# Performance work log

Measured on AMD Instinct MI355X. Metric: run time of the kernel, lower is better.

## Reference

```python
import jax, jax.numpy as jnp
import numpy as np

H = 4  # num_heads in all three MultiheadAttention layers


def _mha(x, valid, Wq, Wk, Wv, Wo, bq, bk, bv, bo):
    """Batched self-attention with key_padding_mask, matching torch MHA math.
    x: [..., L, D]; valid: [..., L] float (1=real token, 0=pad)."""
    lead = x.shape[:-2]
    L, D = x.shape[-2], x.shape[-1]
    dh = D // H
    q = (x @ Wq + bq).reshape(*lead, L, H, dh)
    k = (x @ Wk + bk).reshape(*lead, L, H, dh)
    v = (x @ Wv + bv).reshape(*lead, L, H, dh)
    scores = jnp.einsum('...qhd,...khd->...hqk', q, k) / jnp.sqrt(jnp.asarray(dh, x.dtype))
    neg = jnp.asarray(-1e9, x.dtype)  # finite so fully-masked rows stay NaN-free
    scores = jnp.where(valid[..., None, None, :] > 0, scores, neg)
    a = jax.nn.softmax(scores, axis=-1)
    o = jnp.einsum('...hqk,...khd->...qhd', a, v).reshape(*lead, L, D)
    return o @ Wo + bo


def _masked_mean(x, m):
    # (x * m).sum over sequence / (m.sum + 1e-10); fully-masked -> exact zeros,
    # matching the torch zeros() fallback branch.
    mm = m[..., None]
    return (x * mm).sum(-2) / (mm.sum(-2) + 1e-10)


def setup_inputs() -> dict:
    key = jax.random.key(0)
    B, S, N, W, D = 16, 8, 16, 64, 256
    ks = jax.random.split(key, 16)
    inp = {
        'word_embeddings': jax.random.normal(ks[0], (B, S, N, W, D), dtype=jnp.float32),
        'attention_mask': jax.random.randint(ks[1], (B, S, N, W), 0, 2).astype(jnp.int32),
    }
    i = 2
    for lvl in 'wsc':  # word / sentence / section attention params
        for p in ('Wq', 'Wk', 'Wv', 'Wo'):
            inp[lvl + p] = 0.02 * jax.random.normal(ks[i], (D, D), dtype=jnp.float32)
            i += 1
        for p in ('bq', 'bk', 'bv', 'bo'):
            inp[lvl + p] = jnp.zeros((D,), jnp.float32)
    return inp


def reference(word_embeddings, attention_mask,
              wWq, wWk, wWv, wWo, wbq, wbk, wbv, wbo,
              sWq, sWk, sWv, sWo, sbq, sbk, sbv, sbo,
              cWq, cWk, cWv, cWo, cbq, cbk, cbv, cbo):
    dt = word_embeddings.dtype
    mask = attention_mask.astype(dt)                       # [B,S,N,W]
    # word level: attention within each sentence, then masked mean pooling
    wo = _mha(word_embeddings, mask, wWq, wWk, wWv, wWo, wbq, wbk, wbv, wbo)
    sent = _masked_mean(wo, mask)                          # [B,S,N,D]
    # sentence level
    sent_mask = (mask.sum(-1) > 0).astype(dt)              # [B,S,N]
    so = _mha(sent, sent_mask, sWq, sWk, sWv, sWo, sbq, sbk, sbv, sbo)
    sec = _masked_mean(so, sent_mask)                      # [B,S,D]
    # section level
    sec_mask = (mask.sum((-1, -2)) > 0).astype(dt)         # [B,S]
    co = _mha(sec, sec_mask, cWq, cWk, cWv, cWo, cbq, cbk, cbv, cbo)
    doc = _masked_mean(co, sec_mask)                       # [B,D]
    return doc
```

## Files before the change

kernel.cpp:

```cpp
#include <hip/hip_runtime.h>

constexpr int D = 256;

typedef __attribute__((ext_vector_type(8))) __bf16 bf16x8;
typedef __attribute__((ext_vector_type(4))) float f32x4;
typedef __attribute__((ext_vector_type(16))) float f32x16;

__device__ inline unsigned short f2b(float f) {
    unsigned u = __builtin_bit_cast(unsigned, f);
    u = (u + 0x7fffu + ((u >> 16) & 1u)) >> 16;
    return (unsigned short)u;
}
__device__ inline unsigned cvt_pk_bf16(float lo, float hi) {
    unsigned r;
    asm volatile("v_cvt_pk_bf16_f32 %0, %1, %2" : "=v"(r) : "v"(lo), "v"(hi));
    return r;
}
__device__ inline bf16x8 ld_frag(const void* p) {
    uint4 r = *(const uint4*)p;
    return __builtin_bit_cast(bf16x8, r);
}
__device__ inline bf16x8 mk_frag(unsigned d0, unsigned d1, unsigned d2, unsigned d3) {
    uint4 r = {d0, d1, d2, d3};
    return __builtin_bit_cast(bf16x8, r);
}
template<int CTRL>
__device__ inline float dpp_f(float v) {
    return __builtin_bit_cast(float,
        __builtin_amdgcn_update_dpp(0, __builtin_bit_cast(int, v), CTRL, 0xf, 0xf, true));
}
__device__ inline float rsum16(float v) {
    v += dpp_f<0x121>(v);
    v += dpp_f<0x122>(v);
    v += dpp_f<0x124>(v);
    v += dpp_f<0x128>(v);
    return v;
}
__device__ inline float rmax16(float v) {
    v = fmaxf(v, dpp_f<0x121>(v));
    v = fmaxf(v, dpp_f<0x122>(v));
    v = fmaxf(v, dpp_f<0x124>(v));
    v = fmaxf(v, dpp_f<0x128>(v));
    return v;
}
constexpr float CE = 0.125f * 1.44269504f;

__global__ void prep_wt3(const float* __restrict__ q0, const float* __restrict__ k0,
                         const float* __restrict__ q1, const float* __restrict__ k1,
                         const float* __restrict__ q2, const float* __restrict__ k2,
                         unsigned short* __restrict__ WT) {
    const int b = blockIdx.x, k = threadIdx.x;
    const int lvl = b >> 9, c = b & 511;
    const float* Wq = (lvl == 0) ? q0 : (lvl == 1) ? q1 : q2;
    const float* Wk = (lvl == 0) ? k0 : (lvl == 1) ? k1 : k2;
    const float* W = (c < 256) ? Wq : Wk;
    WT[(size_t)b * 256 + k] = f2b(W[k * 256 + (c & 255)]);
}

__global__ __launch_bounds__(512, 4)
void word_attn(const float* __restrict__ X, const int* __restrict__ Mask,
               const unsigned short* __restrict__ WT,
               const float* __restrict__ bq, const float* __restrict__ bk,
               float* __restrict__ Zout, float* __restrict__ Cnt)
{
    __shared__ unsigned short sX[64 * 256];
    __shared__ unsigned short sK[64 * 256];
    __shared__ float sM[64];
    __shared__ float sAbarT[64][4];
    __shared__ float sCt;

    const int tid = threadIdx.x;
    const int blk = blockIdx.x;
    const float* Xs = X + (size_t)blk * 64 * D;
    char* sXb = (char*)sX;
    char* sKb = (char*)sK;
    const int lane = tid & 63, w = tid >> 6;
    const int l31 = lane & 31, hi = lane >> 5;

    {
        const float4* X4 = (const float4*)Xs;
        float4 xv[8];
        #pragma unroll
        for (int j = 0; j < 8; ++j) xv[j] = X4[tid + j * 512];
        if (tid < 64) sM[tid] = (float)Mask[(size_t)blk * 64 + tid];
        #pragma unroll
        for (int j = 0; j < 8; ++j) {
            uint2 p;
            p.x = cvt_pk_bf16(xv[j].x, xv[j].y);
            p.y = cvt_pk_bf16(xv[j].z, xv[j].w);
            const int row = w + 8 * j;
            *(uint2*)(sXb + row * 512 + ((lane * 8) ^ ((row & 7) << 4))) = p;
        }
    }
    const unsigned short* wtp = WT + (size_t)(w * 64 + l31) * 256 + hi * 8;
    bf16x8 aA[2], aB[2], aC[2], aD[2], b0[2], b1[2];
#define LDA(buf, kkv) { buf[0] = ld_frag(wtp + (kkv) * 16); buf[1] = ld_frag(wtp + 8192 + (kkv) * 16); }
#define LDB(buf, kkv) { \
        buf[0] = ld_frag(sXb + l31 * 512 + (((kkv) * 32 + hi * 16) ^ ((l31 & 7) << 4))); \
        buf[1] = ld_frag(sXb + (32 + l31) * 512 + (((kkv) * 32 + hi * 16) ^ ((l31 & 7) << 4))); }
    LDA(aA, 0); LDA(aB, 1); LDA(aC, 2);
    __syncthreads();
    if (tid < 64) {
        float v = sM[tid];
        #pragma unroll
        for (int o = 1; o < 64; o <<= 1) v += __shfl_xor(v, o);
        if (tid == 0) sCt = v;
    }

    f32x16 acc[2][2];
    {
        const float* bias = (w < 4) ? bq : bk;
        const int fb = (w & 3) * 64;
        #pragma unroll
        for (int mf = 0; mf < 2; ++mf)
            #pragma unroll
            for (int g = 0; g < 4; ++g) {
                float4 b4 = *(const float4*)(bias + fb + mf * 32 + 8 * g + 4 * hi);
                #pragma unroll
                for (int nt = 0; nt < 2; ++nt) {
                    acc[mf][nt][4 * g + 0] = b4.x;
                    acc[mf][nt][4 * g + 1] = b4.y;
                    acc[mf][nt][4 * g + 2] = b4.z;
                    acc[mf][nt][4 * g + 3] = b4.w;
                }
            }
#define MFMA4(a, b) { \
        acc[0][0] = __builtin_amdgcn_mfma_f32_32x32x16_bf16(a[0], b[0], acc[0][0], 0, 0, 0); \
        acc[0][1] = __builtin_amdgcn_mfma_f32_32x32x16_bf16(a[0], b[1], acc[0][1], 0, 0, 0); \
        acc[1][0] = __builtin_amdgcn_mfma_f32_32x32x16_bf16(a[1], b[0], acc[1][0], 0, 0, 0); \
        acc[1][1] = __builtin_amdgcn_mfma_f32_32x32x16_bf16(a[1], b[1], acc[1][1], 0, 0, 0); }
#define PSTEP(ab, bb, an, ka, bn, kb, da, db) { \
        if (da) LDA(an, ka); \
        if (db) LDB(bn, kb); \
        __builtin_amdgcn_s_setprio(1); \
        MFMA4(ab, bb); \
        __builtin_amdgcn_s_setprio(0); }
        LDB(b0, 0);
        PSTEP(aA, b0, aD,  3, b1,  1, 1, 1);
        PSTEP(aB, b1, aA,  4, b0,  2, 1, 1);
        PSTEP(aC, b0, aB,  5, b1,  3, 1, 1);
        PSTEP(aD, b1, aC,  6, b0,  4, 1, 1);
        PSTEP(aA, b0, aD,  7, b1,  5, 1, 1);
        PSTEP(aB, b1, aA,  8, b0,  6, 1, 1);
        PSTEP(aC, b0, aB,  9, b1,  7, 1, 1);
        PSTEP(aD, b1, aC, 10, b0,  8, 1, 1);
        PSTEP(aA, b0, aD, 11, b1,  9, 1, 1);
        PSTEP(aB, b1, aA, 12, b0, 10, 1, 1);
        PSTEP(aC, b0, aB, 13, b1, 11, 1, 1);
        PSTEP(aD, b1, aC, 14, b0, 12, 1, 1);
        PSTEP(aA, b0, aD, 15, b1, 13, 1, 1);
        PSTEP(aB, b1, aA,  0, b0, 14, 0, 1);
        PSTEP(aC, b0, aB,  0, b1, 15, 0, 1);
        PSTEP(aD, b1, aC,  0, b0,  0, 0, 0);
    }

    bf16x8 qfrag[4][2];
    if (w < 4) {
        #pragma unroll
        for (int kk = 0; kk < 4; ++kk) {
            const int mf = kk >> 1, r0 = 8 * (kk & 1);
            #pragma unroll
            for (int i = 0; i < 2; ++i)
                qfrag[kk][i] = mk_frag(
                    cvt_pk_bf16(acc[mf][i][r0 + 0], acc[mf][i][r0 + 1]),
                    cvt_pk_bf16(acc[mf][i][r0 + 2], acc[mf][i][r0 + 3]),
                    cvt_pk_bf16(acc[mf][i][r0 + 4], acc[mf][i][r0 + 5]),
                    cvt_pk_bf16(acc[mf][i][r0 + 6], acc[mf][i][r0 + 7]));
        }
    } else {
        #pragma unroll
        for (int nt = 0; nt < 2; ++nt) {
            const int t = nt * 32 + l31;
            char* rowp = sKb + t * 512;
            const int sw = (t & 7) << 4;
            #pragma unroll
            for (int mf = 0; mf < 2; ++mf)
                #pragma unroll
                for (int g = 0; g < 4; ++g) {
                    uint2 v;
                    v.x = cvt_pk_bf16(acc[mf][nt][4 * g + 0], acc[mf][nt][4 * g + 1]);
                    v.y = cvt_pk_bf16(acc[mf][nt][4 * g + 2], acc[mf][nt][4 * g + 3]);
                    const int fbyte = (w & 3) * 128 + 64 * mf + 32 * (g >> 1) + 16 * hi + 8 * (g & 1);
                    *(uint2*)(rowp + (fbyte ^ sw)) = v;
                }
        }
    }
    __syncthreads();

    if (w < 4) {
        const int h = w;
        f32x16 sc00 = {}, sc01 = {}, sc10 = {}, sc11 = {};
        #pragma unroll
        for (int kk = 0; kk < 4; ++kk) {
            const int fby = h * 128 + kk * 32 + hi * 16;
            bf16x8 kb0 = ld_frag(sKb + l31 * 512 + (fby ^ ((l31 & 7) << 4)));
            bf16x8 kb1 = ld_frag(sKb + (32 + l31) * 512 + (fby ^ ((l31 & 7) << 4)));
            __builtin_amdgcn_s_setprio(1);
            sc00 = __builtin_amdgcn_mfma_f32_32x32x16_bf16(qfrag[kk][0], kb0, sc00, 0, 0, 0);
            sc01 = __builtin_amdgcn_mfma_f32_32x32x16_bf16(qfrag[kk][0], kb1, sc01, 0, 0, 0);
            sc10 = __builtin_amdgcn_mfma_f32_32x32x16_bf16(qfrag[kk][1], kb0, sc10, 0, 0, 0);
            sc11 = __builtin_amdgcn_mfma_f32_32x32x16_bf16(qfrag[kk][1], kb1, sc11, 0, 0, 0);
            __builtin_amdgcn_s_setprio(0);
        }
        const bool k0ok = sM[l31] > 0.f, k1ok = sM[32 + l31] > 0.f;
        float pm0 = 0.f, pm1 = 0.f;
#define SMROW(SC0, SC1, itile) { \
        _Pragma("unroll") \
        for (int r = 0; r < 16; ++r) { \
            const int qrow = 32 * (itile) + (r & 3) + 8 * (r >> 2) + 4 * hi; \
            float e0 = k0ok ? __builtin_amdgcn_exp2f(SC0[r] * CE) : 0.f; \
            float e1 = k1ok ? __builtin_amdgcn_exp2f(SC1[r] * CE) : 0.f; \
            float se = rsum16(e0 + e1); \
            se += __shfl_xor(se, 16); \
            const float wr = sM[qrow] * __builtin_amdgcn_rcpf(se); \
            pm0 += e0 * wr; pm1 += e1 * wr; } }
        SMROW(sc00, sc01, 0)
        SMROW(sc10, sc11, 1)
#undef SMROW
        pm0 += __shfl_xor(pm0, 32);
        pm1 += __shfl_xor(pm1, 32);
        if (hi == 0) {
            sAbarT[l31][h] = pm0;
            sAbarT[32 + l31][h] = pm1;
        }
    }
    uint2 xz[8];
    #pragma unroll
    for (int j = 0; j < 8; ++j) {
        const int t = w + 8 * j;
        xz[j] = *(const uint2*)(sXb + t * 512 + ((lane * 8) ^ ((t & 7) << 4)));
    }
    __syncthreads();

    float zp[4][4];
    #pragma unroll
    for (int h = 0; h < 4; ++h)
        #pragma unroll
        for (int e = 0; e < 4; ++e) zp[h][e] = 0.f;
    #pragma unroll
    for (int j = 0; j < 8; ++j) {
        const int t = w + 8 * j;
        f32x4 ab = *(const f32x4*)&sAbarT[t][0];
        float x0 = __builtin_bit_cast(float, xz[j].x << 16);
        float x1 = __builtin_bit_cast(float, xz[j].x & 0xffff0000u);
        float x2 = __builtin_bit_cast(float, xz[j].y << 16);
        float x3 = __builtin_bit_cast(float, xz[j].y & 0xffff0000u);
        #pragma unroll
        for (int h = 0; h < 4; ++h) {
            zp[h][0] = fmaf(ab[h], x0, zp[h][0]);
            zp[h][1] = fmaf(ab[h], x1, zp[h][1]);
            zp[h][2] = fmaf(ab[h], x2, zp[h][2]);
            zp[h][3] = fmaf(ab[h], x3, zp[h][3]);
        }
    }
    float* zr = (float*)sKb;
    #pragma unroll
    for (int h = 0; h < 4; ++h)
        *(f32x4*)&zr[(w * 4 + h) * 256 + lane * 4] =
            (f32x4){zp[h][0], zp[h][1], zp[h][2], zp[h][3]};
    __syncthreads();
    {
        const int d = tid & 255, hp = (tid >> 8) * 2;
        float a0 = 0.f, a1 = 0.f;
        #pragma unroll
        for (int ww = 0; ww < 8; ++ww) {
            a0 += zr[(ww * 4 + hp) * 256 + d];
            a1 += zr[(ww * 4 + hp + 1) * 256 + d];
        }
        float* Zo = Zout + (size_t)blk * 1024;
        Zo[hp * 256 + d] = a0;
        Zo[(hp + 1) * 256 + d] = a1;
    }
    if (tid == 0) Cnt[blk] = sCt;
#undef LDA
#undef LDB
#undef MFMA4
#undef PSTEP
}

__global__ __launch_bounds__(512, 2)
void apply2(const float* __restrict__ Z, const float* __restrict__ Cnt,
            const float* __restrict__ Wv, const float* __restrict__ Wo,
            const float* __restrict__ bv, const float* __restrict__ bo,
            float* __restrict__ Out, float* __restrict__ MaskOut)
{
    constexpr int SPB = 8;
    __shared__ float sZ[SPB][4][256];
    __shared__ float sPP[SPB][256];
    __shared__ float sH[2][SPB][256];
    __shared__ float sCt[SPB];

    const int tid = threadIdx.x;
    const int s0 = blockIdx.x * SPB;
    {
        const float4* Zf = (const float4*)(Z + (size_t)s0 * 1024);
        float4* sZf = (float4*)sZ;
        #pragma unroll
        for (int k = 0; k < 4; ++k) sZf[tid + k * 512] = Zf[tid + k * 512];
        if (tid < SPB) sCt[tid] = Cnt[s0 + tid];
    }
    __syncthreads();

    const int n = tid & 255, g = tid >> 8, h = n >> 6;

    {
        float pa[SPB] = {};
        for (int dc = 0; dc < 128; dc += 16) {
            float wv[16];
            #pragma unroll
            for (int q = 0; q < 16; ++q) wv[q] = Wv[(size_t)(g * 128 + dc + q) * 256 + n];
            #pragma unroll
            for (int s = 0; s < SPB; ++s) {
                const float4* zp4 = (const float4*)&sZ[s][h][g * 128 + dc];
                #pragma unroll
                for (int q4 = 0; q4 < 4; ++q4) {
                    float4 zv = zp4[q4];
                    pa[s] = fmaf(zv.x, wv[q4 * 4 + 0], pa[s]);
                    pa[s] = fmaf(zv.y, wv[q4 * 4 + 1], pa[s]);
                    pa[s] = fmaf(zv.z, wv[q4 * 4 + 2], pa[s]);
                    pa[s] = fmaf(zv.w, wv[q4 * 4 + 3], pa[s]);
                }
            }
        }
        #pragma unroll
        for (int s = 0; s < SPB; ++s) sH[g][s][n] = pa[s];
    }
    __syncthreads();
    for (int i = tid; i < SPB * 256; i += 512) {
        int s = i >> 8, nn = i & 255;
        sPP[s][nn] = sH[0][s][nn] + sH[1][s][nn] + sCt[s] * bv[nn];
    }
    __syncthreads();
    {
        float pa[SPB] = {};
        for (int dc = 0; dc < 128; dc += 16) {
            float wo[16];
            #pragma unroll
            for (int q = 0; q < 16; ++q) wo[q] = Wo[(size_t)(g * 128 + dc + q) * 256 + n];
            #pragma unroll
            for (int s = 0; s < SPB; ++s) {
                const float4* pp = (const float4*)&sPP[s][g * 128 + dc];
                #pragma unroll
                for (int q4 = 0; q4 < 4; ++q4) {
                    float4 pv = pp[q4];
                    pa[s] = fmaf(pv.x, wo[q4 * 4 + 0], pa[s]);
                    pa[s] = fmaf(pv.y, wo[q4 * 4 + 1], pa[s]);
                    pa[s] = fmaf(pv.z, wo[q4 * 4 + 2], pa[s]);
                    pa[s] = fmaf(pv.w, wo[q4 * 4 + 3], pa[s]);
                }
            }
        }
        #pragma unroll
        for (int s = 0; s < SPB; ++s) sH[g][s][n] = pa[s];
    }
    __syncthreads();
    for (int i = tid; i < SPB * 256; i += 512) {
        int s = i >> 8, nn = i & 255;
        float c = sCt[s];
        Out[(size_t)(s0 + s) * 256 + nn] = (c > 0.f) ? ((sH[0][s][nn] + sH[1][s][nn]) / c + bo[nn]) : 0.f;
    }
    if (tid < SPB && MaskOut) MaskOut[s0 + tid] = (sCt[tid] > 0.f) ? 1.f : 0.f;
}

template<int LREAL>
__global__ __launch_bounds__(512, 2)
void tail_kernel(const float* __restrict__ X, const float* __restrict__ MaskIn,
                 const unsigned short* __restrict__ WT,
                 const float* __restrict__ bq, const float* __restrict__ bk,
                 const float* __restrict__ Wv, const float* __restrict__ Wo,
                 const float* __restrict__ bv, const float* __restrict__ bo,
                 float* __restrict__ Out, float* __restrict__ MaskOut)
{
    __shared__ unsigned short sX[16 * 256];
    __shared__ unsigned short sQK[16 * 512];
    __shared__ float sXF[16][256];
    __shared__ float sM[16];
    __shared__ float sAbar[4][16];
    __shared__ float sZp[2][4][256];
    __shared__ float sPP[256];
    __shared__ float sHH[2][256];
    __shared__ float sCt;

    const int tid = threadIdx.x;
    const int seq = blockIdx.x;
    const float* Xs = X + (size_t)seq * LREAL * 256;
    char* sBX = (char*)sX;
    char* sBQ = (char*)sQK;
    const int lane = tid & 63, w = tid >> 6;
    const int lr = lane & 15, lg = lane >> 4;

    {
        const float4* X4 = (const float4*)Xs;
        #pragma unroll
        for (int j = 0; j < 2; ++j) {
            int idx = tid + j * 512;
            int row = idx >> 6, c4 = idx & 63;
            float4 v = (row < LREAL) ? X4[row * 64 + c4] : (float4){0.f, 0.f, 0.f, 0.f};
            uint2 p;
            p.x = cvt_pk_bf16(v.x, v.y);
            p.y = cvt_pk_bf16(v.z, v.w);
            *(uint2*)(sBX + row * 512 + ((c4 * 8) ^ ((row & 7) << 4))) = p;
            *(float4*)&sXF[row][c4 * 4] = v;
        }
        if (tid < 16) sM[tid] = (tid < LREAL) ? MaskIn[seq * LREAL + tid] : 0.f;
    }
    const unsigned short* wtp = WT + (size_t)(w * 64 + lr) * 256 + lg * 8;
    bf16x8 afn[4];
    #pragma unroll
    for (int m = 0; m < 4; ++m) afn[m] = ld_frag(wtp + m * 16 * 256);
    __syncthreads();
    if (tid < 64) {
        float v = (lane < LREAL) ? sM[lane] : 0.f;
        v = rsum16(v);
        if (lane == 0) sCt = v;
    }

    f32x4 acc[4];
    {
        const float* bias = (w < 4) ? bq : bk;
        const int fb = (w & 3) * 64;
        #pragma unroll
        for (int m = 0; m < 4; ++m) {
            float4 b4 = *(const float4*)(bias + fb + m * 16 + lg * 4);
            acc[m] = (f32x4){b4.x, b4.y, b4.z, b4.w};
        }
        #pragma unroll 1
        for (int kk = 0; kk < 8; ++kk) {
            bf16x8 af[4];
            #pragma unroll
            for (int m = 0; m < 4; ++m) af[m] = afn[m];
            if (kk < 7) {
                #pragma unroll
                for (int m = 0; m < 4; ++m) afn[m] = ld_frag(wtp + m * 16 * 256 + (kk + 1) * 32);
            }
            bf16x8 bx = ld_frag(sBX + lr * 512 + ((kk * 64 + lg * 16) ^ ((lr & 7) << 4)));
            #pragma unroll
            for (int m = 0; m < 4; ++m)
                acc[m] = __builtin_amdgcn_mfma_f32_16x16x32_bf16(af[m], bx, acc[m], 0, 0, 0);
        }
    }
    #pragma unroll
    for (int m = 0; m < 4; ++m) {
        uint2 qk;
        qk.x = cvt_pk_bf16(acc[m][0], acc[m][1]);
        qk.y = cvt_pk_bf16(acc[m][2], acc[m][3]);
        *(uint2*)(sBQ + lr * 1024 + ((w * 128 + m * 32 + lg * 8) ^ ((lr & 7) << 4))) = qk;
    }
    __syncthreads();

    if (w < 4) {
        const int h = w;
        f32x4 sacc = (f32x4){0.f, 0.f, 0.f, 0.f};
        #pragma unroll
        for (int kk = 0; kk < 2; ++kk) {
            bf16x8 qf = ld_frag(sBQ + lr * 1024 + ((h * 128 + kk * 64 + lg * 16) ^ ((lr & 7) << 4)));
            bf16x8 kf = ld_frag(sBQ + lr * 1024 + ((512 + h * 128 + kk * 64 + lg * 16) ^ ((lr & 7) << 4)));
            sacc = __builtin_amdgcn_mfma_f32_16x16x32_bf16(qf, kf, sacc, 0, 0, 0);
        }
        const float mkey = sM[lr];
        float t = 0.f;
        #pragma unroll
        for (int r = 0; r < 4; ++r) {
            const int qi = lg * 4 + r;
            float s = (mkey > 0.f) ? sacc[r] : -1e9f;
            float mx = rmax16(s);
            float e = __builtin_amdgcn_exp2f((s - mx) * CE);
            float se = rsum16(e);
            t += e * (sM[qi] * __builtin_amdgcn_rcpf(se));
        }
        t += __shfl_xor(t, 16);
        t += __shfl_xor(t, 32);
        if (lane < 16) sAbar[h][lane] = t;
    }
    __syncthreads();

    {
        const int d = tid & 255, rh = tid >> 8;
        float zz[4] = {0.f, 0.f, 0.f, 0.f};
        #pragma unroll
        for (int t = 0; t < 8; ++t) {
            const int tok = rh * 8 + t;
            float xv = sXF[tok][d];
            #pragma unroll
            for (int h = 0; h < 4; ++h) zz[h] = fmaf(sAbar[h][tok], xv, zz[h]);
        }
        #pragma unroll
        for (int h = 0; h < 4; ++h) sZp[rh][h][d] = zz[h];
    }
    __syncthreads();

    const int n = tid & 255, g = tid >> 8, h = n >> 6;
    {
        float pa = 0.f;
        for (int dc = 0; dc < 128; dc += 16) {
            float wv[16];
            #pragma unroll
            for (int q = 0; q < 16; ++q) wv[q] = Wv[(size_t)(g * 128 + dc + q) * 256 + n];
            #pragma unroll
            for (int q = 0; q < 16; ++q) {
                int dd = g * 128 + dc + q;
                pa = fmaf(sZp[0][h][dd] + sZp[1][h][dd], wv[q], pa);
            }
        }
        sHH[g][n] = pa;
    }
    __syncthreads();
    if (tid < 256) sPP[tid] = sHH[0][tid] + sHH[1][tid] + sCt * bv[tid];
    __syncthreads();
    {
        float pa = 0.f;
        for (int dc = 0; dc < 128; dc += 16) {
            float wo[16];
            #pragma unroll
            for (int q = 0; q < 16; ++q) wo[q] = Wo[(size_t)(g * 128 + dc + q) * 256 + n];
            const float* pp = &sPP[g * 128 + dc];
            #pragma unroll
            for (int q = 0; q < 16; ++q) pa = fmaf(pp[q], wo[q], pa);
        }
        sHH[g][n] = pa;
    }
    __syncthreads();
    if (tid < 256) {
        float c = sCt;
        Out[(size_t)seq * 256 + tid] = (c > 0.f) ? ((sHH[0][tid] + sHH[1][tid]) / c + bo[tid]) : 0.f;
        if (MaskOut && tid == 0) MaskOut[seq] = (c > 0.f) ? 1.f : 0.f;
    }
}

extern "C" void kernel_launch(void* const* d_in, const int* in_sizes, int n_in,
                              void* d_out, int out_size, void* d_ws, size_t ws_size,
                              hipStream_t stream)
{
    const float* emb  = (const float*)d_in[0];
    const int*  amask = (const int*)d_in[1];
    const float* W[24];
    for (int i = 0; i < 24; ++i) W[i] = (const float*)d_in[2 + i];

    char* ws = (char*)d_ws;
    unsigned short* WT = (unsigned short*)ws;
    float* zbuf  = (float*)(ws + 3 * 256 * 1024);
    float* cnt   = zbuf + 2048 * 1024;
    float* sent  = cnt + 2048;
    float* smask = sent + 2048 * 256;
    float* sec   = smask + 2048;
    float* cmask = sec + 128 * 256;
    float* out   = (float*)d_out;

    prep_wt3<<<dim3(1536), dim3(256), 0, stream>>>(W[0], W[1], W[8], W[9], W[16], W[17], WT);

    word_attn<<<dim3(2048), dim3(512), 0, stream>>>(emb, amask, WT, W[4], W[5], zbuf, cnt);
    apply2<<<dim3(256), dim3(512), 0, stream>>>(zbuf, cnt, W[2], W[3], W[6], W[7], sent, smask);

    tail_kernel<16><<<dim3(128), dim3(512), 0, stream>>>(
        sent, smask, WT + 512 * 256, W[12], W[13], W[10], W[11], W[14], W[15], sec, cmask);

    tail_kernel<8><<<dim3(16), dim3(512), 0, stream>>>(
        sec, cmask, WT + 2 * 512 * 256, W[20], W[21], W[18], W[19], W[22], W[23], out, nullptr);
}
```

Before: 148.2 us.

## Make word_attn persistent over four sequences with register prefetch of next input

```diff
diff --git a/kernel.cpp b/kernel.cpp
--- a/kernel.cpp
+++ b/kernel.cpp
@@ -67,63 +67,19 @@
     __shared__ unsigned short sK[64 * 256];
     __shared__ float sM[64];
     __shared__ float sAbarT[64][4];
-    __shared__ float sCt;
 
     const int tid = threadIdx.x;
-    const int blk = blockIdx.x;
-    const float* Xs = X + (size_t)blk * 64 * D;
+    const int lane = tid & 63, w = tid >> 6;
+    const int l31 = lane & 31, hi = lane >> 5;
     char* sXb = (char*)sX;
     char* sKb = (char*)sK;
-    const int lane = tid & 63, w = tid >> 6;
-    const int l31 = lane & 31, hi = lane >> 5;
-
-    {
-        const float4* X4 = (const float4*)Xs;
-        float4 xv[8];
-        #pragma unroll
-        for (int j = 0; j < 8; ++j) xv[j] = X4[tid + j * 512];
-        if (tid < 64) sM[tid] = (float)Mask[(size_t)blk * 64 + tid];
-        #pragma unroll
-        for (int j = 0; j < 8; ++j) {
-            uint2 p;
-            p.x = cvt_pk_bf16(xv[j].x, xv[j].y);
-            p.y = cvt_pk_bf16(xv[j].z, xv[j].w);
-            const int row = w + 8 * j;
-            *(uint2*)(sXb + row * 512 + ((lane * 8) ^ ((row & 7) << 4))) = p;
-        }
-    }
+
     const unsigned short* wtp = WT + (size_t)(w * 64 + l31) * 256 + hi * 8;
     bf16x8 aA[2], aB[2], aC[2], aD[2], b0[2], b1[2];
 #define LDA(buf, kkv) { buf[0] = ld_frag(wtp + (kkv) * 16); buf[1] = ld_frag(wtp + 8192 + (kkv) * 16); }
 #define LDB(buf, kkv) { \
         buf[0] = ld_frag(sXb + l31 * 512 + (((kkv) * 32 + hi * 16) ^ ((l31 & 7) << 4))); \
         buf[1] = ld_frag(sXb + (32 + l31) * 512 + (((kkv) * 32 + hi * 16) ^ ((l31 & 7) << 4))); }
-    LDA(aA, 0); LDA(aB, 1); LDA(aC, 2);
-    __syncthreads();
-    if (tid < 64) {
-        float v = sM[tid];
-        #pragma unroll
-        for (int o = 1; o < 64; o <<= 1) v += __shfl_xor(v, o);
-        if (tid == 0) sCt = v;
-    }
-
-    f32x16 acc[2][2];
-    {
-        const float* bias = (w < 4) ? bq : bk;
-        const int fb = (w & 3) * 64;
-        #pragma unroll
-        for (int mf = 0; mf < 2; ++mf)
-            #pragma unroll
-            for (int g = 0; g < 4; ++g) {
-                float4 b4 = *(const float4*)(bias + fb + mf * 32 + 8 * g + 4 * hi);
-                #pragma unroll
-                for (int nt = 0; nt < 2; ++nt) {
-                    acc[mf][nt][4 * g + 0] = b4.x;
-                    acc[mf][nt][4 * g + 1] = b4.y;
-                    acc[mf][nt][4 * g + 2] = b4.z;
-                    acc[mf][nt][4 * g + 3] = b4.w;
-                }
-            }
 #define MFMA4(a, b) { \
         acc[0][0] = __builtin_amdgcn_mfma_f32_32x32x16_bf16(a[0], b[0], acc[0][0], 0, 0, 0); \
         acc[0][1] = __builtin_amdgcn_mfma_f32_32x32x16_bf16(a[0], b[1], acc[0][1], 0, 0, 0); \
@@ -135,143 +91,200 @@
         __builtin_amdgcn_s_setprio(1); \
         MFMA4(ab, bb); \
         __builtin_amdgcn_s_setprio(0); }
-        LDB(b0, 0);
-        PSTEP(aA, b0, aD,  3, b1,  1, 1, 1);
-        PSTEP(aB, b1, aA,  4, b0,  2, 1, 1);
-        PSTEP(aC, b0, aB,  5, b1,  3, 1, 1);
-        PSTEP(aD, b1, aC,  6, b0,  4, 1, 1);
-        PSTEP(aA, b0, aD,  7, b1,  5, 1, 1);
-        PSTEP(aB, b1, aA,  8, b0,  6, 1, 1);
-        PSTEP(aC, b0, aB,  9, b1,  7, 1, 1);
-        PSTEP(aD, b1, aC, 10, b0,  8, 1, 1);
-        PSTEP(aA, b0, aD, 11, b1,  9, 1, 1);
-        PSTEP(aB, b1, aA, 12, b0, 10, 1, 1);
-        PSTEP(aC, b0, aB, 13, b1, 11, 1, 1);
-        PSTEP(aD, b1, aC, 14, b0, 12, 1, 1);
-        PSTEP(aA, b0, aD, 15, b1, 13, 1, 1);
-        PSTEP(aB, b1, aA,  0, b0, 14, 0, 1);
-        PSTEP(aC, b0, aB,  0, b1, 15, 0, 1);
-        PSTEP(aD, b1, aC,  0, b0,  0, 0, 0);
-    }
-
-    bf16x8 qfrag[4][2];
-    if (w < 4) {
-        #pragma unroll
-        for (int kk = 0; kk < 4; ++kk) {
-            const int mf = kk >> 1, r0 = 8 * (kk & 1);
-            #pragma unroll
-            for (int i = 0; i < 2; ++i)
-                qfrag[kk][i] = mk_frag(
-                    cvt_pk_bf16(acc[mf][i][r0 + 0], acc[mf][i][r0 + 1]),
-                    cvt_pk_bf16(acc[mf][i][r0 + 2], acc[mf][i][r0 + 3]),
-                    cvt_pk_bf16(acc[mf][i][r0 + 4], acc[mf][i][r0 + 5]),
-                    cvt_pk_bf16(acc[mf][i][r0 + 6], acc[mf][i][r0 + 7]));
-        }
-    } else {
-        #pragma unroll
-        for (int nt = 0; nt < 2; ++nt) {
-            const int t = nt * 32 + l31;
-            char* rowp = sKb + t * 512;
-            const int sw = (t & 7) << 4;
+
+    int seq = blockIdx.x * 4;
+    float4 xv[8];
+    float mv = 0.f;
+    {
+        const float4* X4 = (const float4*)(X + (size_t)seq * 64 * D);
+        #pragma unroll
+        for (int j = 0; j < 8; ++j) xv[j] = X4[tid + j * 512];
+        if (tid < 64) mv = (float)Mask[(size_t)seq * 64 + tid];
+    }
+    LDA(aA, 0); LDA(aB, 1); LDA(aC, 2);
+
+    #pragma unroll 1
+    for (int it = 0; it < 4; ++it) {
+        #pragma unroll
+        for (int j = 0; j < 8; ++j) {
+            uint2 p;
+            p.x = cvt_pk_bf16(xv[j].x, xv[j].y);
+            p.y = cvt_pk_bf16(xv[j].z, xv[j].w);
+            const int row = w + 8 * j;
+            *(uint2*)(sXb + row * 512 + ((lane * 8) ^ ((row & 7) << 4))) = p;
+        }
+        if (tid < 64) sM[tid] = mv;
+        __syncthreads();
+        if (tid < 64) {
+            float v = sM[tid];
+            #pragma unroll
+            for (int o = 1; o < 64; o <<= 1) v += __shfl_xor(v, o);
+            if (tid == 0) Cnt[seq] = v;
+        }
+
+        f32x16 acc[2][2];
+        {
+            const float* bias = (w < 4) ? bq : bk;
+            const int fb = (w & 3) * 64;
             #pragma unroll
             for (int mf = 0; mf < 2; ++mf)
                 #pragma unroll
                 for (int g = 0; g < 4; ++g) {
-                    uint2 v;
-                    v.x = cvt_pk_bf16(acc[mf][nt][4 * g + 0], acc[mf][nt][4 * g + 1]);
-                    v.y = cvt_pk_bf16(acc[mf][nt][4 * g + 2], acc[mf][nt][4 * g + 3]);
-                    const int fbyte = (w & 3) * 128 + 64 * mf + 32 * (g >> 1) + 16 * hi + 8 * (g & 1);
-                    *(uint2*)(rowp + (fbyte ^ sw)) = v;
+                    float4 b4 = *(const float4*)(bias + fb + mf * 32 + 8 * g + 4 * hi);
+                    #pragma unroll
+                    for (int nt = 0; nt < 2; ++nt) {
+                        acc[mf][nt][4 * g + 0] = b4.x;
+                        acc[mf][nt][4 * g + 1] = b4.y;
+                        acc[mf][nt][4 * g + 2] = b4.z;
+                        acc[mf][nt][4 * g + 3] = b4.w;
+                    }
                 }
-        }
-    }
-    __syncthreads();
-
-    if (w < 4) {
-        const int h = w;
-        f32x16 sc00 = {}, sc01 = {}, sc10 = {}, sc11 = {};
-        #pragma unroll
-        for (int kk = 0; kk < 4; ++kk) {
-            const int fby = h * 128 + kk * 32 + hi * 16;
-            bf16x8 kb0 = ld_frag(sKb + l31 * 512 + (fby ^ ((l31 & 7) << 4)));
-            bf16x8 kb1 = ld_frag(sKb + (32 + l31) * 512 + (fby ^ ((l31 & 7) << 4)));
-            __builtin_amdgcn_s_setprio(1);
-            sc00 = __builtin_amdgcn_mfma_f32_32x32x16_bf16(qfrag[kk][0], kb0, sc00, 0, 0, 0);
-            sc01 = __builtin_amdgcn_mfma_f32_32x32x16_bf16(qfrag[kk][0], kb1, sc01, 0, 0, 0);
-            sc10 = __builtin_amdgcn_mfma_f32_32x32x16_bf16(qfrag[kk][1], kb0, sc10, 0, 0, 0);
-            sc11 = __builtin_amdgcn_mfma_f32_32x32x16_bf16(qfrag[kk][1], kb1, sc11, 0, 0, 0);
-            __builtin_amdgcn_s_setprio(0);
-        }
-        const bool k0ok = sM[l31] > 0.f, k1ok = sM[32 + l31] > 0.f;
-        float pm0 = 0.f, pm1 = 0.f;
+            LDB(b0, 0);
+            PSTEP(aA, b0, aD,  3, b1,  1, 1, 1);
+            PSTEP(aB, b1, aA,  4, b0,  2, 1, 1);
+            PSTEP(aC, b0, aB,  5, b1,  3, 1, 1);
+            PSTEP(aD, b1, aC,  6, b0,  4, 1, 1);
+            PSTEP(aA, b0, aD,  7, b1,  5, 1, 1);
+            PSTEP(aB, b1, aA,  8, b0,  6, 1, 1);
+            PSTEP(aC, b0, aB,  9, b1,  7, 1, 1);
+            PSTEP(aD, b1, aC, 10, b0,  8, 1, 1);
+            PSTEP(aA, b0, aD, 11, b1,  9, 1, 1);
+            PSTEP(aB, b1, aA, 12, b0, 10, 1, 1);
+            PSTEP(aC, b0, aB, 13, b1, 11, 1, 1);
+            PSTEP(aD, b1, aC, 14, b0, 12, 1, 1);
+            PSTEP(aA, b0, aD, 15, b1, 13, 1, 1);
+            PSTEP(aB, b1, aA,  0, b0, 14, 0, 1);
+            PSTEP(aC, b0, aB,  0, b1, 15, 0, 1);
+            PSTEP(aD, b1, aC,  0, b0,  0, 0, 0);
+        }
+
+        bf16x8 qfrag[4][2];
+        if (w < 4) {
+            #pragma unroll
+            for (int kk = 0; kk < 4; ++kk) {
+                const int mf = kk >> 1, r0 = 8 * (kk & 1);
+                #pragma unroll
+                for (int i = 0; i < 2; ++i)
+                    qfrag[kk][i] = mk_frag(
+                        cvt_pk_bf16(acc[mf][i][r0 + 0], acc[mf][i][r0 + 1]),
+                        cvt_pk_bf16(acc[mf][i][r0 + 2], acc[mf][i][r0 + 3]),
+                        cvt_pk_bf16(acc[mf][i][r0 + 4], acc[mf][i][r0 + 5]),
+                        cvt_pk_bf16(acc[mf][i][r0 + 6], acc[mf][i][r0 + 7]));
+            }
+        } else {
+            #pragma unroll
+            for (int nt = 0; nt < 2; ++nt) {
+                const int t = nt * 32 + l31;
+                char* rowp = sKb + t * 512;
+                const int sw = (t & 7) << 4;
+                #pragma unroll
+                for (int mf = 0; mf < 2; ++mf)
+                    #pragma unroll
+                    for (int g = 0; g < 4; ++g) {
+                        uint2 v;
+                        v.x = cvt_pk_bf16(acc[mf][nt][4 * g + 0], acc[mf][nt][4 * g + 1]);
+                        v.y = cvt_pk_bf16(acc[mf][nt][4 * g + 2], acc[mf][nt][4 * g + 3]);
+                        const int fbyte = (w & 3) * 128 + 64 * mf + 32 * (g >> 1) + 16 * hi + 8 * (g & 1);
+                        *(uint2*)(rowp + (fbyte ^ sw)) = v;
+                    }
+            }
+        }
+        __syncthreads();
+
+        if (w < 4) {
+            const int h = w;
+            f32x16 sc00 = {}, sc01 = {}, sc10 = {}, sc11 = {};
+            #pragma unroll
+            for (int kk = 0; kk < 4; ++kk) {
+                const int fby = h * 128 + kk * 32 + hi * 16;
+                bf16x8 kb0 = ld_frag(sKb + l31 * 512 + (fby ^ ((l31 & 7) << 4)));
+                bf16x8 kb1 = ld_frag(sKb + (32 + l31) * 512 + (fby ^ ((l31 & 7) << 4)));
+                __builtin_amdgcn_s_setprio(1);
+                sc00 = __builtin_amdgcn_mfma_f32_32x32x16_bf16(qfrag[kk][0], kb0, sc00, 0, 0, 0);
+                sc01 = __builtin_amdgcn_mfma_f32_32x32x16_bf16(qfrag[kk][0], kb1, sc01, 0, 0, 0);
+                sc10 = __builtin_amdgcn_mfma_f32_32x32x16_bf16(qfrag[kk][1], kb0, sc10, 0, 0, 0);
+                sc11 = __builtin_amdgcn_mfma_f32_32x32x16_bf16(qfrag[kk][1], kb1, sc11, 0, 0, 0);
+                __builtin_amdgcn_s_setprio(0);
+            }
+            const bool k0ok = sM[l31] > 0.f, k1ok = sM[32 + l31] > 0.f;
+            float pm0 = 0.f, pm1 = 0.f;
 #define SMROW(SC0, SC1, itile) { \
-        _Pragma("unroll") \
-        for (int r = 0; r < 16; ++r) { \
-            const int qrow = 32 * (itile) + (r & 3) + 8 * (r >> 2) + 4 * hi; \
-            float e0 = k0ok ? __builtin_amdgcn_exp2f(SC0[r] * CE) : 0.f; \
-            float e1 = k1ok ? __builtin_amdgcn_exp2f(SC1[r] * CE) : 0.f; \
-            float se = rsum16(e0 + e1); \
-            se += __shfl_xor(se, 16); \
-            const float wr = sM[qrow] * __builtin_amdgcn_rcpf(se); \
-            pm0 += e0 * wr; pm1 += e1 * wr; } }
-        SMROW(sc00, sc01, 0)
-        SMROW(sc10, sc11, 1)
+            _Pragma("unroll") \
+            for (int r = 0; r < 16; ++r) { \
+                const int qrow = 32 * (itile) + (r & 3) + 8 * (r >> 2) + 4 * hi; \
+                float e0 = k0ok ? __builtin_amdgcn_exp2f(SC0[r] * CE) : 0.f; \
+                float e1 = k1ok ? __builtin_amdgcn_exp2f(SC1[r] * CE) : 0.f; \
+                float se = rsum16(e0 + e1); \
+                se += __shfl_xor(se, 16); \
+                const float wr = sM[qrow] * __builtin_amdgcn_rcpf(se); \
+                pm0 += e0 * wr; pm1 += e1 * wr; } }
+            SMROW(sc00, sc01, 0)
+            SMROW(sc10, sc11, 1)
 #undef SMROW
-        pm0 += __shfl_xor(pm0, 32);
-        pm1 += __shfl_xor(pm1, 32);
-        if (hi == 0) {
-            sAbarT[l31][h] = pm0;
-            sAbarT[32 + l31][h] = pm1;
-        }
-    }
-    uint2 xz[8];
-    #pragma unroll
-    for (int j = 0; j < 8; ++j) {
-        const int t = w + 8 * j;
-        xz[j] = *(const uint2*)(sXb + t * 512 + ((lane * 8) ^ ((t & 7) << 4)));
-    }
-    __syncthreads();
-
-    float zp[4][4];
-    #pragma unroll
-    for (int h = 0; h < 4; ++h)
-        #pragma unroll
-        for (int e = 0; e < 4; ++e) zp[h][e] = 0.f;
-    #pragma unroll
-    for (int j = 0; j < 8; ++j) {
-        const int t = w + 8 * j;
-        f32x4 ab = *(const f32x4*)&sAbarT[t][0];
-        float x0 = __builtin_bit_cast(float, xz[j].x << 16);
-        float x1 = __builtin_bit_cast(float, xz[j].x & 0xffff0000u);
-        float x2 = __builtin_bit_cast(float, xz[j].y << 16);
-        float x3 = __builtin_bit_cast(float, xz[j].y & 0xffff0000u);
-        #pragma unroll
-        for (int h = 0; h < 4; ++h) {
-            zp[h][0] = fmaf(ab[h], x0, zp[h][0]);
-            zp[h][1] = fmaf(ab[h], x1, zp[h][1]);
-            zp[h][2] = fmaf(ab[h], x2, zp[h][2]);
-            zp[h][3] = fmaf(ab[h], x3, zp[h][3]);
-        }
-    }
-    float* zr = (float*)sKb;
-    #pragma unroll
-    for (int h = 0; h < 4; ++h)
-        *(f32x4*)&zr[(w * 4 + h) * 256 + lane * 4] =
-            (f32x4){zp[h][0], zp[h][1], zp[h][2], zp[h][3]};
-    __syncthreads();
-    {
-        const int d = tid & 255, hp = (tid >> 8) * 2;
-        float a0 = 0.f, a1 = 0.f;
-        #pragma unroll
-        for (int ww = 0; ww < 8; ++ww) {
-            a0 += zr[(ww * 4 + hp) * 256 + d];
-            a1 += zr[(ww * 4 + hp + 1) * 256 + d];
-        }
-        float* Zo = Zout + (size_t)blk * 1024;
-        Zo[hp * 256 + d] = a0;
-        Zo[(hp + 1) * 256 + d] = a1;
-    }
-    if (tid == 0) Cnt[blk] = sCt;
+            pm0 += __shfl_xor(pm0, 32);
+            pm1 += __shfl_xor(pm1, 32);
+            if (hi == 0) {
+                sAbarT[l31][w] = pm0;
+                sAbarT[32 + l31][w] = pm1;
+            }
+        }
+        uint2 xz[8];
+        #pragma unroll
+        for (int j = 0; j < 8; ++j) {
+            const int t = w + 8 * j;
+            xz[j] = *(const uint2*)(sXb + t * 512 + ((lane * 8) ^ ((t & 7) << 4)));
+        }
+        __syncthreads();
+
+        if (it < 3) {
+            const float4* Xn = (const float4*)(X + (size_t)(seq + 1) * 64 * D);
+            #pragma unroll
+            for (int j = 0; j < 8; ++j) xv[j] = Xn[tid + j * 512];
+            if (tid < 64) mv = (float)Mask[(size_t)(seq + 1) * 64 + tid];
+        }
+
+        float zp[4][4];
+        #pragma unroll
+        for (int h = 0; h < 4; ++h)
+            #pragma unroll
+            for (int e = 0; e < 4; ++e) zp[h][e] = 0.f;
+        #pragma unroll
+        for (int j = 0; j < 8; ++j) {
+            const int t = w + 8 * j;
+            f32x4 ab = *(const f32x4*)&sAbarT[t][0];
+            float x0 = __builtin_bit_cast(float, xz[j].x << 16);
+            float x1 = __builtin_bit_cast(float, xz[j].x & 0xffff0000u);
+            float x2 = __builtin_bit_cast(float, xz[j].y << 16);
+            float x3 = __builtin_bit_cast(float, xz[j].y & 0xffff0000u);
+            #pragma unroll
+            for (int h = 0; h < 4; ++h) {
+                zp[h][0] = fmaf(ab[h], x0, zp[h][0]);
+                zp[h][1] = fmaf(ab[h], x1, zp[h][1]);
+                zp[h][2] = fmaf(ab[h], x2, zp[h][2]);
+                zp[h][3] = fmaf(ab[h], x3, zp[h][3]);
+            }
+        }
+        float* zr = (float*)sKb;
+        #pragma unroll
+        for (int h = 0; h < 4; ++h)
+            *(f32x4*)&zr[(w * 4 + h) * 256 + lane * 4] =
+                (f32x4){zp[h][0], zp[h][1], zp[h][2], zp[h][3]};
+        __syncthreads();
+        {
+            const int d = tid & 255, hp = (tid >> 8) * 2;
+            float a0 = 0.f, a1 = 0.f;
+            #pragma unroll
+            for (int ww = 0; ww < 8; ++ww) {
+                a0 += zr[(ww * 4 + hp) * 256 + d];
+                a1 += zr[(ww * 4 + hp + 1) * 256 + d];
+            }
+            float* Zo = Zout + (size_t)seq * 1024;
+            Zo[hp * 256 + d] = a0;
+            Zo[(hp + 1) * 256 + d] = a1;
+        }
+        if (it < 3) { LDA(aA, 0); LDA(aB, 1); LDA(aC, 2); }
+        seq += 1;
+    }
 #undef LDA
 #undef LDB
 #undef MFMA4
@@ -548,7 +561,7 @@
 
     prep_wt3<<<dim3(1536), dim3(256), 0, stream>>>(W[0], W[1], W[8], W[9], W[16], W[17], WT);
 
-    word_attn<<<dim3(2048), dim3(512), 0, stream>>>(emb, amask, WT, W[4], W[5], zbuf, cnt);
+    word_attn<<<dim3(512), dim3(512), 0, stream>>>(emb, amask, WT, W[4], W[5], zbuf, cnt);
     apply2<<<dim3(256), dim3(512), 0, stream>>>(zbuf, cnt, W[2], W[3], W[6], W[7], sent, smask);
 
     tail_kernel<16><<<dim3(128), dim3(512), 0, stream>>>(
```

Measured after the change: 281.9 us. 1.9x slower.

## Fuse word-level output projection with sentence-level attention into one kernel

Applied to the files above, without the earlier changes.

```diff
diff --git a/kernel.cpp b/kernel.cpp
--- a/kernel.cpp
+++ b/kernel.cpp
@@ -279,87 +279,228 @@
 }
 
 __global__ __launch_bounds__(512, 2)
-void apply2(const float* __restrict__ Z, const float* __restrict__ Cnt,
-            const float* __restrict__ Wv, const float* __restrict__ Wo,
-            const float* __restrict__ bv, const float* __restrict__ bo,
-            float* __restrict__ Out, float* __restrict__ MaskOut)
+void sent_fused(const float* __restrict__ Z, const float* __restrict__ Cnt,
+                const float* __restrict__ wWv, const float* __restrict__ wWo,
+                const float* __restrict__ wbv, const float* __restrict__ wbo,
+                const unsigned short* __restrict__ WT,
+                const float* __restrict__ bq, const float* __restrict__ bk,
+                const float* __restrict__ sWv, const float* __restrict__ sWo,
+                const float* __restrict__ sbv, const float* __restrict__ sbo,
+                float* __restrict__ Out, float* __restrict__ MaskOut)
 {
-    constexpr int SPB = 8;
-    __shared__ float sZ[SPB][4][256];
-    __shared__ float sPP[SPB][256];
-    __shared__ float sH[2][SPB][256];
-    __shared__ float sCt[SPB];
+    __shared__ __align__(16) unsigned char uni[65536];
+    __shared__ float sM[16];
+    __shared__ float sAbar[4][16];
+    __shared__ float sCt16[16];
+    __shared__ float sCt;
 
     const int tid = threadIdx.x;
-    const int s0 = blockIdx.x * SPB;
-    {
-        const float4* Zf = (const float4*)(Z + (size_t)s0 * 1024);
-        float4* sZf = (float4*)sZ;
-        #pragma unroll
-        for (int k = 0; k < 4; ++k) sZf[tid + k * 512] = Zf[tid + k * 512];
-        if (tid < SPB) sCt[tid] = Cnt[s0 + tid];
+    const int blk = blockIdx.x;
+    const int lane = tid & 63, w = tid >> 6;
+    const int lr = lane & 15, lg = lane >> 4;
+    float* sXF = (float*)(uni + 49152);
+
+    {
+        float* zQ = (float*)uni;
+        const float4* Zf = (const float4*)(Z + (size_t)blk * 16 * 1024);
+        float4* zQ4 = (float4*)zQ;
+        #pragma unroll
+        for (int k = 0; k < 8; ++k) zQ4[tid + k * 512] = Zf[tid + k * 512];
+        if (tid < 16) sCt16[tid] = Cnt[blk * 16 + tid];
+        __syncthreads();
+
+        const int n = tid & 255, g = tid >> 8, h = n >> 6;
+        float pa[16];
+        #pragma unroll
+        for (int s = 0; s < 16; ++s) pa[s] = 0.f;
+        for (int dc = 0; dc < 128; dc += 8) {
+            float wv[8];
+            #pragma unroll
+            for (int q = 0; q < 8; ++q) wv[q] = wWv[(size_t)(g * 128 + dc + q) * 256 + n];
+            #pragma unroll
+            for (int s = 0; s < 16; ++s) {
+                const float* zp = zQ + s * 1024 + h * 256 + g * 128 + dc;
+                #pragma unroll
+                for (int q = 0; q < 8; ++q) pa[s] = fmaf(zp[q], wv[q], pa[s]);
+            }
+        }
+        __syncthreads();
+        float* sH = (float*)uni;
+        #pragma unroll
+        for (int s = 0; s < 16; ++s) sH[(g * 16 + s) * 256 + n] = pa[s];
+        __syncthreads();
+        float* sPPa = (float*)(uni + 32768);
+        for (int i = tid; i < 4096; i += 512) {
+            int s = i >> 8, nn = i & 255;
+            sPPa[s * 256 + nn] = sH[s * 256 + nn] + sH[(16 + s) * 256 + nn] + sCt16[s] * wbv[nn];
+        }
+        __syncthreads();
+        #pragma unroll
+        for (int s = 0; s < 16; ++s) pa[s] = 0.f;
+        for (int dc = 0; dc < 128; dc += 8) {
+            float wo[8];
+            #pragma unroll
+            for (int q = 0; q < 8; ++q) wo[q] = wWo[(size_t)(g * 128 + dc + q) * 256 + n];
+            #pragma unroll
+            for (int s = 0; s < 16; ++s) {
+                const float* pp = sPPa + s * 256 + g * 128 + dc;
+                #pragma unroll
+                for (int q = 0; q < 8; ++q) pa[s] = fmaf(pp[q], wo[q], pa[s]);
+            }
+        }
+        __syncthreads();
+        #pragma unroll
+        for (int s = 0; s < 16; ++s) sH[(g * 16 + s) * 256 + n] = pa[s];
+        __syncthreads();
+        for (int i = tid; i < 4096; i += 512) {
+            int s = i >> 8, nn = i & 255;
+            float c = sCt16[s];
+            sXF[s * 256 + nn] = (c > 0.f) ? ((sH[s * 256 + nn] + sH[(16 + s) * 256 + nn]) / c + wbo[nn]) : 0.f;
+        }
+        if (tid < 16) sM[tid] = (sCt16[tid] > 0.f) ? 1.f : 0.f;
+        __syncthreads();
+    }
+
+    char* sBX = (char*)uni;
+    char* sBQ = (char*)(uni + 8192);
+    float* sZp = (float*)(uni + 24576);
+    float* sPP2 = (float*)(uni + 32768);
+    float* sHH  = (float*)(uni + 36864);
+
+    {
+        const float4* XF4 = (const float4*)sXF;
+        #pragma unroll
+        for (int j = 0; j < 2; ++j) {
+            int idx = tid + j * 512;
+            int row = idx >> 6, c4 = idx & 63;
+            float4 v = XF4[row * 64 + c4];
+            uint2 p;
+            p.x = cvt_pk_bf16(v.x, v.y);
+            p.y = cvt_pk_bf16(v.z, v.w);
+            *(uint2*)(sBX + row * 512 + ((c4 * 8) ^ ((row & 7) << 4))) = p;
+        }
+    }
+    const unsigned short* wtp = WT + (size_t)(w * 64 + lr) * 256 + lg * 8;
+    bf16x8 afn[4];
+    #pragma unroll
+    for (int m = 0; m < 4; ++m) afn[m] = ld_frag(wtp + m * 16 * 256);
+    __syncthreads();
+    if (tid < 64) {
+        float v = (lane < 16) ? sM[lane] : 0.f;
+        v = rsum16(v);
+        if (lane == 0) sCt = v;
+    }
+
+    f32x4 acc[4];
+    {
+        const float* bias = (w < 4) ? bq : bk;
+        const int fb = (w & 3) * 64;
+        #pragma unroll
+        for (int m = 0; m < 4; ++m) {
+            float4 b4 = *(const float4*)(bias + fb + m * 16 + lg * 4);
+            acc[m] = (f32x4){b4.x, b4.y, b4.z, b4.w};
+        }
+        #pragma unroll 1
+        for (int kk = 0; kk < 8; ++kk) {
+            bf16x8 af[4];
+            #pragma unroll
+            for (int m = 0; m < 4; ++m) af[m] = afn[m];
+            if (kk < 7) {
+                #pragma unroll
+                for (int m = 0; m < 4; ++m) afn[m] = ld_frag(wtp + m * 16 * 256 + (kk + 1) * 32);
+            }
+            bf16x8 bx = ld_frag(sBX + lr * 512 + ((kk * 64 + lg * 16) ^ ((lr & 7) << 4)));
+            #pragma unroll
+            for (int m = 0; m < 4; ++m)
+                acc[m] = __builtin_amdgcn_mfma_f32_16x16x32_bf16(af[m], bx, acc[m], 0, 0, 0);
+        }
+    }
+    #pragma unroll
+    for (int m = 0; m < 4; ++m) {
+        uint2 qk;
+        qk.x = cvt_pk_bf16(acc[m][0], acc[m][1]);
+        qk.y = cvt_pk_bf16(acc[m][2], acc[m][3]);
+        *(uint2*)(sBQ + lr * 1024 + ((w * 128 + m * 32 + lg * 8) ^ ((lr & 7) << 4))) = qk;
+    }
+    __syncthreads();
+
+    if (w < 4) {
+        const int h = w;
+        f32x4 sacc = (f32x4){0.f, 0.f, 0.f, 0.f};
+        #pragma unroll
+        for (int kk = 0; kk < 2; ++kk) {
+            bf16x8 qf = ld_frag(sBQ + lr * 1024 + ((h * 128 + kk * 64 + lg * 16) ^ ((lr & 7) << 4)));
+            bf16x8 kf = ld_frag(sBQ + lr * 1024 + ((512 + h * 128 + kk * 64 + lg * 16) ^ ((lr & 7) << 4)));
+            sacc = __builtin_amdgcn_mfma_f32_16x16x32_bf16(qf, kf, sacc, 0, 0, 0);
+        }
+        const float mkey = sM[lr];
+        float t = 0.f;
+        #pragma unroll
+        for (int r = 0; r < 4; ++r) {
+            const int qi = lg * 4 + r;
+            float s = (mkey > 0.f) ? sacc[r] : -1e9f;
+            float mx = rmax16(s);
+            float e = __builtin_amdgcn_exp2f((s - mx) * CE);
+            float se = rsum16(e);
+            t += e * (sM[qi] * __builtin_amdgcn_rcpf(se));
+        }
+        t += __shfl_xor(t, 16);
+        t += __shfl_xor(t, 32);
+        if (lane < 16) sAbar[h][lane] = t;
+    }
+    __syncthreads();
+
+    {
+        const int d = tid & 255, rh = tid >> 8;
+        float zz[4] = {0.f, 0.f, 0.f, 0.f};
+        #pragma unroll
+        for (int t = 0; t < 8; ++t) {
+            const int tok = rh * 8 + t;
+            float xv = sXF[tok * 256 + d];
+            #pragma unroll
+            for (int h = 0; h < 4; ++h) zz[h] = fmaf(sAbar[h][tok], xv, zz[h]);
+        }
+        #pragma unroll
+        for (int h = 0; h < 4; ++h) sZp[(rh * 4 + h) * 256 + d] = zz[h];
     }
     __syncthreads();
 
     const int n = tid & 255, g = tid >> 8, h = n >> 6;
-
-    {
-        float pa[SPB] = {};
+    {
+        float pa = 0.f;
         for (int dc = 0; dc < 128; dc += 16) {
             float wv[16];
             #pragma unroll
-            for (int q = 0; q < 16; ++q) wv[q] = Wv[(size_t)(g * 128 + dc + q) * 256 + n];
-            #pragma unroll
-            for (int s = 0; s < SPB; ++s) {
-                const float4* zp4 = (const float4*)&sZ[s][h][g * 128 + dc];
-                #pragma unroll
-                for (int q4 = 0; q4 < 4; ++q4) {
-                    float4 zv = zp4[q4];
-                    pa[s] = fmaf(zv.x, wv[q4 * 4 + 0], pa[s]);
-                    pa[s] = fmaf(zv.y, wv[q4 * 4 + 1], pa[s]);
-                    pa[s] = fmaf(zv.z, wv[q4 * 4 + 2], pa[s]);
-                    pa[s] = fmaf(zv.w, wv[q4 * 4 + 3], pa[s]);
-                }
+            for (int q = 0; q < 16; ++q) wv[q] = sWv[(size_t)(g * 128 + dc + q) * 256 + n];
+            #pragma unroll
+            for (int q = 0; q < 16; ++q) {
+                int dd = g * 128 + dc + q;
+                pa = fmaf(sZp[h * 256 + dd] + sZp[(4 + h) * 256 + dd], wv[q], pa);
             }
         }
-        #pragma unroll
-        for (int s = 0; s < SPB; ++s) sH[g][s][n] = pa[s];
-    }
-    __syncthreads();
-    for (int i = tid; i < SPB * 256; i += 512) {
-        int s = i >> 8, nn = i & 255;
-        sPP[s][nn] = sH[0][s][nn] + sH[1][s][nn] + sCt[s] * bv[nn];
-    }
-    __syncthreads();
-    {
-        float pa[SPB] = {};
+        sHH[g * 256 + n] = pa;
+    }
+    __syncthreads();
+    if (tid < 256) sPP2[tid] = sHH[tid] + sHH[256 + tid] + sCt * sbv[tid];
+    __syncthreads();
+    {
+        float pa = 0.f;
         for (int dc = 0; dc < 128; dc += 16) {
             float wo[16];
             #pragma unroll
-            for (int q = 0; q < 16; ++q) wo[q] = Wo[(size_t)(g * 128 + dc + q) * 256 + n];
-            #pragma unroll
-            for (int s = 0; s < SPB; ++s) {
-                const float4* pp = (const float4*)&sPP[s][g * 128 + dc];
-                #pragma unroll
-                for (int q4 = 0; q4 < 4; ++q4) {
-                    float4 pv = pp[q4];
-                    pa[s] = fmaf(pv.x, wo[q4 * 4 + 0], pa[s]);
-                    pa[s] = fmaf(pv.y, wo[q4 * 4 + 1], pa[s]);
-                    pa[s] = fmaf(pv.z, wo[q4 * 4 + 2], pa[s]);
-                    pa[s] = fmaf(pv.w, wo[q4 * 4 + 3], pa[s]);
-                }
-            }
-        }
-        #pragma unroll
-        for (int s = 0; s < SPB; ++s) sH[g][s][n] = pa[s];
-    }
-    __syncthreads();
-    for (int i = tid; i < SPB * 256; i += 512) {
-        int s = i >> 8, nn = i & 255;
-        float c = sCt[s];
-        Out[(size_t)(s0 + s) * 256 + nn] = (c > 0.f) ? ((sH[0][s][nn] + sH[1][s][nn]) / c + bo[nn]) : 0.f;
-    }
-    if (tid < SPB && MaskOut) MaskOut[s0 + tid] = (sCt[tid] > 0.f) ? 1.f : 0.f;
+            for (int q = 0; q < 16; ++q) wo[q] = sWo[(size_t)(g * 128 + dc + q) * 256 + n];
+            const float* pp = sPP2 + g * 128 + dc;
+            #pragma unroll
+            for (int q = 0; q < 16; ++q) pa = fmaf(pp[q], wo[q], pa);
+        }
+        sHH[g * 256 + n] = pa;
+    }
+    __syncthreads();
+    if (tid < 256) {
+        float c = sCt;
+        Out[(size_t)blk * 256 + tid] = (c > 0.f) ? ((sHH[tid] + sHH[256 + tid]) / c + sbo[tid]) : 0.f;
+        if (MaskOut && tid == 0) MaskOut[blk] = (c > 0.f) ? 1.f : 0.f;
+    }
 }
 
 template<int LREAL>
@@ -540,19 +681,17 @@
     unsigned short* WT = (unsigned short*)ws;
     float* zbuf  = (float*)(ws + 3 * 256 * 1024);
     float* cnt   = zbuf + 2048 * 1024;
-    float* sent  = cnt + 2048;
-    float* smask = sent + 2048 * 256;
-    float* sec   = smask + 2048;
+    float* sec   = cnt + 2048;
     float* cmask = sec + 128 * 256;
     float* out   = (float*)d_out;
 
     prep_wt3<<<dim3(1536), dim3(256), 0, stream>>>(W[0], W[1], W[8], W[9], W[16], W[17], WT);
 
     word_attn<<<dim3(2048), dim3(512), 0, stream>>>(emb, amask, WT, W[4], W[5], zbuf, cnt);
-    apply2<<<dim3(256), dim3(512), 0, stream>>>(zbuf, cnt, W[2], W[3], W[6], W[7], sent, smask);
-
-    tail_kernel<16><<<dim3(128), dim3(512), 0, stream>>>(
-        sent, smask, WT + 512 * 256, W[12], W[13], W[10], W[11], W[14], W[15], sec, cmask);
+
+    sent_fused<<<dim3(128), dim3(512), 0, stream>>>(
+        zbuf, cnt, W[2], W[3], W[6], W[7],
+        WT + 512 * 256, W[12], W[13], W[10], W[11], W[14], W[15], sec, cmask);
 
     tail_kernel<8><<<dim3(16), dim3(512), 0, stream>>>(
         sec, cmask, WT + 2 * 512 * 256, W[20], W[21], W[18], W[19], W[22], W[23], out, nullptr);
```

Result: slower. 156.9 us (+5.8%).
